# Performance work log

Hardware: AMD Instinct MI355X
Metric: run time of the kernel (lower is better)

## Reference

```python
import math
import jax, jax.numpy as jnp
import numpy as np

B, DIM, H = 16, 1024, 16
HD = DIM // H                      # 64
P_ORIG = 1024                      # num_patches arg
NP = math.ceil(math.sqrt(P_ORIG)) ** 2 // 2   # 512 attended tokens
ALPHA, BETA, GAMMA = 1.9, 3.8, 15.2           # iRPE euc config, ratio=1.9
NUM_BUCKETS = 2 * int(BETA) + 1               # 7


def _rp_bucket(L):
    """Static euclidean-distance relative-position buckets (iRPE 'euc')."""
    E = int(math.ceil(math.sqrt(L)))
    flat = np.arange(E * E)
    pos = np.stack([flat // E, flat % E], axis=1)[:L].astype(np.float64)  # [L,2]
    diff = pos[:, None, :] - pos[None, :, :]
    dis = np.round(np.sqrt((diff ** 2).sum(-1)))
    far = np.round(ALPHA + np.log(np.maximum(dis, 1e-9) / ALPHA)
                   / math.log(GAMMA / ALPHA) * (BETA - ALPHA))
    idx = np.where(dis <= ALPHA, np.round(dis), np.minimum(far, BETA)).astype(np.int32)
    idx = idx - idx.min()
    return jnp.asarray(idx)  # [L,L] int32 in [0, int(BETA)]

RP_BUCKET = _rp_bucket(NP)


def setup_inputs() -> dict:
    key = jax.random.key(0)
    ks = jax.random.split(key, 7)
    s = 0.02
    return {
        "x": jax.random.normal(ks[0], (B, P_ORIG, DIM), dtype=jnp.float32),
        "wq": jax.random.normal(ks[1], (DIM, DIM), dtype=jnp.float32) * s,
        "wk": jax.random.normal(ks[2], (DIM, DIM), dtype=jnp.float32) * s,
        "wv": jax.random.normal(ks[3], (DIM, DIM), dtype=jnp.float32) * s,
        "rpe_w": jax.random.normal(ks[4], (HD, NUM_BUCKETS), dtype=jnp.float32) * s,
        "proj_w": jax.random.normal(ks[5], (DIM, DIM), dtype=jnp.float32) * s,
        "proj_b": jax.random.normal(ks[6], (DIM,), dtype=jnp.float32) * s,
    }


def reference(x, wq, wk, wv, rpe_w, proj_w, proj_b):
    # F.pad on token axis with pad = NP - N (negative => crop)
    pad = NP - x.shape[1]
    if pad >= 0:
        x = jnp.pad(x, ((0, 0), (0, pad), (0, 0)))
    else:
        x = x[:, :NP, :]
    b = x.shape[0]
    scale = HD ** (-0.5)

    def heads(t):  # [b,NP,DIM] -> [b,H,NP,HD]
        return t.reshape(b, NP, H, HD).transpose(0, 2, 1, 3)

    q = heads(x @ wq.T)
    k = heads(x @ wk.T)
    v = heads(x @ wv.T)

    attn = jnp.einsum('bhid,bhjd->bhij', q, k) * scale
    # contextual RPE on keys (transposed): bias[b,h,i,j] = q[b,h,i,:] . W[:, bucket[i,j]]
    lt = jnp.einsum('bhid,dn->bhin', q, rpe_w)                 # [b,H,NP,NB]
    bias = jnp.take_along_axis(lt, RP_BUCKET[None, None, :, :], axis=3)  # [b,H,NP,NP]
    attn = jax.nn.softmax(attn + bias, axis=-1)

    out = jnp.einsum('bhij,bhjd->bhid', attn, v)
    out = out.transpose(0, 2, 1, 3).reshape(b, NP, DIM)
    out = out @ proj_w.T + proj_b
    return out[:, :P_ORIG, :]
```

## Files before the change

kernel.cpp:

```cpp
#include <hip/hip_runtime.h>

typedef __attribute__((ext_vector_type(8))) __bf16 bf16x8;
typedef __attribute__((ext_vector_type(4))) float f32x4;

#define DEVI static __device__ __forceinline__

DEVI unsigned short f2bf(float f) {
  unsigned int u = __float_as_uint(f);
  u += 0x7fffu + ((u >> 16) & 1u);
  return (unsigned short)(u >> 16);
}
DEVI float bf2f(unsigned short s) {
  return __uint_as_float(((unsigned int)s) << 16);
}

union Frag {
  bf16x8 v;
  __bf16 hf[8];
  unsigned short h[8];
  unsigned int w[4];
};

typedef __attribute__((address_space(1))) const void gv_t;
typedef __attribute__((address_space(3))) void sv_t;
#define GLOAD_LDS16(gp, lp) __builtin_amdgcn_global_load_lds((gv_t*)(gp), (sv_t*)(lp), 16, 0, 0)

#define QSCALE 0.18033688011112042f

__global__ __launch_bounds__(256) void k_prep(
    const float* __restrict__ x, const float* __restrict__ wq,
    const float* __restrict__ wk, const float* __restrict__ wv,
    const float* __restrict__ pw,
    unsigned short* __restrict__ xb, unsigned short* __restrict__ wb,
    unsigned char* __restrict__ bkt)
{
  int t = blockIdx.x * 256 + threadIdx.x;
  if (t >= 1572864) {
    int q = t - 1572864;
    int i = q >> 9, j = q & 511;
    int ir = i / 23, ic = i - ir * 23;
    int jr = j / 23, jc = j - jr * 23;
    int dy = ir - jr, dx = ic - jc;
    double dis = rint(sqrt((double)(dy * dy + dx * dx)));
    int v;
    if (dis <= 1.9) {
      v = (int)rint(dis);
    } else {
      double far = rint(1.9 + log(dis / 1.9) * (1.9 / log(8.0)));
      v = (int)fmin(far, 3.8);
    }
    bkt[q] = (unsigned char)v;
    return;
  }
  const float* src;
  unsigned short* dst;
  if (t < 1048576) {
    long e0 = (long)t << 3;
    int m = (int)(e0 >> 10), cc = (int)(e0 & 1023);
    int b = m >> 9, i = m & 511;
    src = x + (((long)(b << 10) + i) << 10) + cc;
    dst = xb + ((long)m << 10) + cc;
  } else {
    long e0 = (long)(t - 1048576) << 3;
    int mat = (int)(e0 >> 20);
    long off = e0 & 1048575;
    const float* s = (mat == 0) ? wq : (mat == 1) ? wk : (mat == 2) ? wv : pw;
    src = s + off;
    dst = wb + e0;
  }
  float4 a = *(const float4*)src;
  float4 b4 = *(const float4*)(src + 4);
  uint4 o;
  o.x = f2bf(a.x)  | ((unsigned)f2bf(a.y)  << 16);
  o.y = f2bf(a.z)  | ((unsigned)f2bf(a.w)  << 16);
  o.z = f2bf(b4.x) | ((unsigned)f2bf(b4.y) << 16);
  o.w = f2bf(b4.z) | ((unsigned)f2bf(b4.w) << 16);
  *(uint4*)dst = o;
}

__global__ __launch_bounds__(512) void k_gemm8(
    const unsigned short* __restrict__ A,
    const unsigned short* __restrict__ Bw,
    unsigned short* __restrict__ qh, unsigned short* __restrict__ kh,
    unsigned short* __restrict__ vt)
{
  __shared__ unsigned short sL[2 * 28672];

  const int bid = blockIdx.x;
  const int swz = (bid & 7) * 64 + (bid >> 3);
  const int tileN = swz & 15, tileM = swz >> 4;

  const int t = threadIdx.x;
  const int w = t >> 6, lane = t & 63;
  const int g4 = lane >> 4, c = lane & 15;
  const int wm = w >> 2, wn = w & 3;

  const char* lbase = (const char*)sL;
  const int acb = c * 64 + ((g4 * 16) ^ ((c & 8) ? 32 : 0));
  const int aoffbase = wm * 8192 + acb;
  int boff[3][2];
#pragma unroll
  for (int ni = 0; ni < 3; ++ni) {
    int row = wn * 48 + ni * 16 + c;
    int base = 32768 + (row >> 6) * 8192 + (row & 63) * 128;
    int rx = row & 7;
#pragma unroll
    for (int kk = 0; kk < 2; ++kk)
      boff[ni][kk] = base + (((kk * 4 + g4) ^ rx) << 4);
  }

  const int rowa = w * 16 + (lane >> 2);
  const int cola = ((lane & 3) * 8) ^ (((lane >> 2) & 8) ? 16 : 0);
  const unsigned short* sAp = A + (long)(tileM * 256 + rowa) * 1024 + cola;
  char* ldsta = (char*)sL + t * 16;
  const int rowbb = t >> 3;
  const int colbb = ((t & 7) ^ ((t >> 3) & 7)) * 8;
  const unsigned short* sBp = Bw + (long)(tileN * 192 + rowbb) * 1024 + colbb;
  char* ldstb = (char*)sL + 32768 + t * 16;

#define STGA(rh, kh, kn, ob) \
  GLOAD_LDS16(sAp + (long)(kn) * 64 + (rh) * 131072 + (kh) * 32, \
              ldsta + (ob) + (kh) * 16384 + (rh) * 8192)
#define STGB(gg, kn, ob) \
  GLOAD_LDS16(sBp + (long)(kn) * 64 + (gg) * 65536, \
              ldstb + (ob) + (gg) * 8192)

  f32x4 acc[8][3] = {};

  STGA(0, 0, 0, 0); STGA(1, 0, 0, 0);
  STGB(0, 0, 0); STGB(1, 0, 0); STGB(2, 0, 0);
  STGA(0, 1, 0, 0); STGA(1, 1, 0, 0);

#pragma unroll 1
  for (int kt = 0; kt < 16; ++kt) {
    const int cb = (kt & 1) ? 57344 : 0;
    const int ob = cb ^ 57344;
    const int kn = (kt < 15) ? kt + 1 : 15;

    {
      asm volatile("s_waitcnt vmcnt(2)" ::: "memory");
      __builtin_amdgcn_s_barrier();
      bf16x8 aa[4], bbf[3];
#pragma unroll
      for (int q = 0; q < 4; ++q)
        aa[q] = *(const bf16x8*)(lbase + cb + aoffbase + q * 1024);
#pragma unroll
      for (int ni = 0; ni < 3; ++ni)
        bbf[ni] = *(const bf16x8*)(lbase + cb + boff[ni][0]);
      STGA(0, 0, kn, ob); STGA(1, 0, kn, ob); STGB(0, kn, ob);
      __builtin_amdgcn_s_setprio(1);
#pragma unroll
      for (int mi = 0; mi < 4; ++mi)
#pragma unroll
        for (int ni = 0; ni < 3; ++ni)
          acc[mi][ni] = __builtin_amdgcn_mfma_f32_16x16x32_bf16(aa[mi], bbf[ni], acc[mi][ni], 0, 0, 0);
      __builtin_amdgcn_s_setprio(0);
      bf16x8 a2[4];
#pragma unroll
      for (int q = 0; q < 4; ++q)
        a2[q] = *(const bf16x8*)(lbase + cb + aoffbase + (4 + q) * 1024);
      STGB(1, kn, ob); STGB(2, kn, ob);
      __builtin_amdgcn_s_setprio(1);
#pragma unroll
      for (int mi = 0; mi < 4; ++mi)
#pragma unroll
        for (int ni = 0; ni < 3; ++ni)
          acc[4 + mi][ni] = __builtin_amdgcn_mfma_f32_16x16x32_bf16(a2[mi], bbf[ni], acc[4 + mi][ni], 0, 0, 0);
      __builtin_amdgcn_s_setprio(0);
    }
    {
      asm volatile("s_waitcnt vmcnt(5)" ::: "memory");
      __builtin_amdgcn_s_barrier();
      bf16x8 aa[4], bbf[3];
#pragma unroll
      for (int q = 0; q < 4; ++q)
        aa[q] = *(const bf16x8*)(lbase + cb + 16384 + aoffbase + q * 1024);
#pragma unroll
      for (int ni = 0; ni < 3; ++ni)
        bbf[ni] = *(const bf16x8*)(lbase + cb + boff[ni][1]);
      STGA(0, 1, kn, ob);
      __builtin_amdgcn_s_setprio(1);
#pragma unroll
      for (int mi = 0; mi < 4; ++mi)
#pragma unroll
        for (int ni = 0; ni < 3; ++ni)
          acc[mi][ni] = __builtin_amdgcn_mfma_f32_16x16x32_bf16(aa[mi], bbf[ni], acc[mi][ni], 0, 0, 0);
      __builtin_amdgcn_s_setprio(0);
      bf16x8 a2[4];
#pragma unroll
      for (int q = 0; q < 4; ++q)
        a2[q] = *(const bf16x8*)(lbase + cb + 16384 + aoffbase + (4 + q) * 1024);
      STGA(1, 1, kn, ob);
      __builtin_amdgcn_s_setprio(1);
#pragma unroll
      for (int mi = 0; mi < 4; ++mi)
#pragma unroll
        for (int ni = 0; ni < 3; ++ni)
          acc[4 + mi][ni] = __builtin_amdgcn_mfma_f32_16x16x32_bf16(a2[mi], bbf[ni], acc[4 + mi][ni], 0, 0, 0);
      __builtin_amdgcn_s_setprio(0);
    }
  }
  asm volatile("s_waitcnt vmcnt(0)" ::: "memory");
#undef STGA
#undef STGB

  const int m0 = tileM * 256 + wm * 128;
  const int n0 = tileN * 192 + wn * 48;
#pragma unroll
  for (int mi = 0; mi < 8; ++mi) {
    int mrow = m0 + mi * 16 + g4 * 4;
    int b = mrow >> 9, i = mrow & 511;
#pragma unroll
    for (int ni = 0; ni < 3; ++ni) {
      int n = n0 + ni * 16 + c;
      int mat = n >> 10;
      int cc = n & 1023;
      int h = cc >> 6, d = cc & 63;
      long bh = (long)(b * 16 + h);
      if (mat == 2) {
        unsigned int w0 = f2bf(acc[mi][ni][0]) | ((unsigned)f2bf(acc[mi][ni][1]) << 16);
        unsigned int w1 = f2bf(acc[mi][ni][2]) | ((unsigned)f2bf(acc[mi][ni][3]) << 16);
        *(uint2*)(vt + (bh * 64 + d) * 512 + i) = make_uint2(w0, w1);
      } else {
        float sc = (mat == 0) ? QSCALE : 1.0f;
        unsigned short* dst = (mat == 0 ? qh : kh) + (bh * 512 + i) * 64 + d;
#pragma unroll
        for (int r = 0; r < 4; ++r)
          dst[(long)r * 64] = f2bf(acc[mi][ni][r] * sc);
      }
    }
  }
}

__global__ __launch_bounds__(512) void k_gemm_proj(
    const unsigned short* __restrict__ A,
    const unsigned short* __restrict__ Bw,
    float* __restrict__ out, const float* __restrict__ bias)
{
  __shared__ unsigned short sL[3 * 12288];

  const int bid = blockIdx.x;
  const int swz = (bid & 7) * 32 + (bid >> 3);
  const int tileN = swz % 8, tileM = swz / 8;

  const int tid = threadIdx.x;
  const int w = tid >> 6, lane = tid & 63;
  const int g = lane >> 4, c = lane & 15;
  const int wm = w >> 1, wn = w & 1;

  const int sk = (g * 8) ^ ((c & 8) ? 16 : 0);
  int offA[4], offB[4];
#pragma unroll
  for (int i = 0; i < 4; ++i) {
    offA[i] = (wm * 4 + i) * 512 + c * 32 + sk;
    offB[i] = 8192 + (wn * 4 + i) * 512 + c * 32 + sk;
  }

  const int colb = ((lane & 3) * 8) ^ ((lane >= 32) ? 16 : 0);
  const unsigned short* gA0 = A  + ((long)(tileM * 256 + w * 32 + (lane >> 2))) * 1024 + colb;
  const unsigned short* gA1 = gA0 + 16 * 1024;
  const unsigned short* gB0 = Bw + ((long)(tileN * 128 + w * 16 + (lane >> 2))) * 1024 + colb;

#define STAGE(ktile, buf) do {                                             \
    const long ko_ = (long)(ktile) * 32;                                   \
    char* base_ = (char*)sL + (buf) * 24576;                               \
    GLOAD_LDS16(gA0 + ko_, base_ + (w * 2) * 1024 + lane * 16);            \
    GLOAD_LDS16(gA1 + ko_, base_ + (w * 2 + 1) * 1024 + lane * 16);        \
    GLOAD_LDS16(gB0 + ko_, base_ + 16384 + w * 1024 + lane * 16);          \
  } while (0)

  f32x4 acc[4][4] = {};

  STAGE(0, 0);
  STAGE(1, 1);

  int rb = 0, wbuf = 2;
  for (int t = 0; t < 32; ++t) {
    asm volatile("s_waitcnt vmcnt(3)" ::: "memory");
    __builtin_amdgcn_s_barrier();
    int kt = t + 2; if (kt > 31) kt = 31;
    STAGE(kt, wbuf);

    const unsigned short* lb = sL + rb * 12288;
    bf16x8 af[4], bf[4];
#pragma unroll
    for (int i = 0; i < 4; ++i) af[i] = *(const bf16x8*)(lb + offA[i]);
#pragma unroll
    for (int i = 0; i < 4; ++i) bf[i] = *(const bf16x8*)(lb + offB[i]);

    __builtin_amdgcn_s_setprio(1);
#pragma unroll
    for (int mi = 0; mi < 4; ++mi)
#pragma unroll
      for (int ni = 0; ni < 4; ++ni)
        acc[mi][ni] = __builtin_amdgcn_mfma_f32_16x16x32_bf16(af[mi], bf[ni], acc[mi][ni], 0, 0, 0);
    __builtin_amdgcn_s_setprio(0);
    asm volatile("s_waitcnt lgkmcnt(0)" ::: "memory");

    rb = (rb == 2) ? 0 : rb + 1;
    wbuf = (wbuf == 2) ? 0 : wbuf + 1;
  }
  asm volatile("s_waitcnt vmcnt(0)" ::: "memory");
#undef STAGE

  const int m0 = tileM * 256 + wm * 64;
  const int n0 = tileN * 128 + wn * 64;
#pragma unroll
  for (int mi = 0; mi < 4; ++mi) {
    int mrow = m0 + mi * 16 + g * 4;
#pragma unroll
    for (int ni = 0; ni < 4; ++ni) {
      int n = n0 + ni * 16 + c;
      float bv = bias[n];
#pragma unroll
      for (int r = 0; r < 4; ++r)
        out[(long)(mrow + r) * 1024 + n] = acc[mi][ni][r] + bv;
    }
  }
}

__global__ __launch_bounds__(512) void k_attn(
    const unsigned short* __restrict__ qh, const unsigned short* __restrict__ kh,
    const unsigned short* __restrict__ vt, const float* __restrict__ rpe,
    const unsigned char* __restrict__ bkt, unsigned short* __restrict__ ao)
{
  __shared__ float lt_lds[512 * 9];
  const int head = blockIdx.x;
  const int b = head >> 4, h = head & 15;
  const int w = threadIdx.x >> 6, lane = threadIdx.x & 63;
  const int g = lane >> 4, c = lane & 15;
  const int qbase = w * 64;
  const unsigned short* Q = qh + (long)head * 512 * 64;
  const unsigned short* K = kh + (long)head * 512 * 64;
  const unsigned short* V = vt + (long)head * 64 * 512;

  Frag qu[4][2];
#pragma unroll
  for (int it = 0; it < 4; ++it)
#pragma unroll
    for (int kk = 0; kk < 2; ++kk)
      qu[it][kk].v = *(const bf16x8*)(Q + (qbase + it * 16 + c) * 64 + kk * 32 + g * 8);

  float lt[4][7] = {};
#pragma unroll
  for (int kk = 0; kk < 2; ++kk)
#pragma unroll
    for (int tt = 0; tt < 8; ++tt) {
      int d = kk * 32 + g * 8 + tt;
      const float* rr = rpe + d * 7;
      float r0 = rr[0], r1 = rr[1], r2 = rr[2], r3 = rr[3], r4 = rr[4], r5 = rr[5], r6 = rr[6];
#pragma unroll
      for (int it = 0; it < 4; ++it) {
        float qv = bf2f(qu[it][kk].h[tt]);
        lt[it][0] += qv * r0; lt[it][1] += qv * r1; lt[it][2] += qv * r2;
        lt[it][3] += qv * r3; lt[it][4] += qv * r4; lt[it][5] += qv * r5;
        lt[it][6] += qv * r6;
      }
    }
#pragma unroll
  for (int it = 0; it < 4; ++it)
#pragma unroll
    for (int n = 0; n < 7; ++n) {
      float v = lt[it][n];
      v += __shfl_xor(v, 16);
      v += __shfl_xor(v, 32);
      if (g == 0) lt_lds[(qbase + it * 16 + c) * 9 + n] = v * 8.0f;
    }

  int rowb36[4];
  const unsigned char* bktp[4];
#pragma unroll
  for (int it = 0; it < 4; ++it) {
    int row = qbase + it * 16 + c;
    rowb36[it] = row * 36;
    bktp[it] = bkt + (long)row * 512 + g * 8;
  }

  f32x4 oacc[4][4] = {};
  float lp[4] = {0.f, 0.f, 0.f, 0.f};
  const int jperm = (c >> 2) * 8 + (c & 3);

  for (int jb = 0; jb < 512; jb += 32) {
    const int jp0 = jb + jperm;
    Frag kf[2][2];
#pragma unroll
    for (int jt = 0; jt < 2; ++jt)
#pragma unroll
      for (int kk = 0; kk < 2; ++kk)
        kf[jt][kk].v = *(const bf16x8*)(K + (jp0 + jt * 4) * 64 + kk * 32 + g * 8);

    uint2 bb[4];
#pragma unroll
    for (int it = 0; it < 4; ++it)
      bb[it] = *(const uint2*)(bktp[it] + jb);

    f32x4 s[2][4];
#pragma unroll
    for (int jt = 0; jt < 2; ++jt)
#pragma unroll
      for (int it = 0; it < 4; ++it) {
        f32x4 z = {0.f, 0.f, 0.f, 0.f};
        z = __builtin_amdgcn_mfma_f32_16x16x32_bf16(kf[jt][0].v, qu[it][0].v, z, 0, 0, 0);
        s[jt][it] = __builtin_amdgcn_mfma_f32_16x16x32_bf16(kf[jt][1].v, qu[it][1].v, z, 0, 0, 0);
      }

    Frag pfr[4];
#pragma unroll
    for (int it = 0; it < 4; ++it) {
      float ps = 0.f;
#pragma unroll
      for (int jt = 0; jt < 2; ++jt) {
        unsigned int bw = jt ? bb[it].y : bb[it].x;
#pragma unroll
        for (int r = 0; r < 4; ++r) {
          int bno = (bw >> (8 * r)) & 255;
          float bias = *(const float*)((const char*)lt_lds + rowb36[it] + (bno << 2));
          float sv = s[jt][it][r] + bias;
          float p;
          asm("v_exp_f32 %0, %1" : "=v"(p) : "v"(sv));
          ps += p;
          pfr[it].hf[jt * 4 + r] = (__bf16)p;
        }
      }
      lp[it] += ps;
    }

    bf16x8 vf[4];
#pragma unroll
    for (int dt = 0; dt < 4; ++dt)
      vf[dt] = *(const bf16x8*)(V + (dt * 16 + c) * 512 + jb + g * 8);

#pragma unroll
    for (int dt = 0; dt < 4; ++dt)
#pragma unroll
      for (int it = 0; it < 4; ++it)
        oacc[dt][it] = __builtin_amdgcn_mfma_f32_16x16x32_bf16(vf[dt], pfr[it].v, oacc[dt][it], 0, 0, 0);
  }

  float li[4];
#pragma unroll
  for (int it = 0; it < 4; ++it) {
    float v = lp[it];
    v += __shfl_xor(v, 16);
    v += __shfl_xor(v, 32);
    li[it] = 1.0f / v;
  }
#pragma unroll
  for (int dt = 0; dt < 4; ++dt)
#pragma unroll
    for (int it = 0; it < 4; ++it) {
      int irow = qbase + it * 16 + c;
      int d0 = dt * 16 + g * 4;
      unsigned int w0 = f2bf(oacc[dt][it][0] * li[it]) | ((unsigned)f2bf(oacc[dt][it][1] * li[it]) << 16);
      unsigned int w1 = f2bf(oacc[dt][it][2] * li[it]) | ((unsigned)f2bf(oacc[dt][it][3] * li[it]) << 16);
      *(uint2*)(ao + ((long)(b * 512 + irow)) * 1024 + h * 64 + d0) = make_uint2(w0, w1);
    }
}

extern "C" void kernel_launch(void* const* d_in, const int* in_sizes, int n_in,
                              void* d_out, int out_size, void* d_ws, size_t ws_size,
                              hipStream_t stream) {
  const float* x   = (const float*)d_in[0];
  const float* wq  = (const float*)d_in[1];
  const float* wk  = (const float*)d_in[2];
  const float* wv  = (const float*)d_in[3];
  const float* rpe = (const float*)d_in[4];
  const float* pw  = (const float*)d_in[5];
  const float* pb  = (const float*)d_in[6];
  float* out = (float*)d_out;

  char* ws = (char*)d_ws;
  unsigned short* xb  = (unsigned short*)(ws);
  unsigned short* wb  = (unsigned short*)(ws + 16777216);
  unsigned short* qhp = (unsigned short*)(ws + 25165824);
  unsigned short* khp = (unsigned short*)(ws + 41943040);
  unsigned short* vtp = (unsigned short*)(ws + 58720256);
  unsigned char*  bkt = (unsigned char*)(ws + 75497472);
  unsigned short* aop = xb;

  k_prep<<<dim3(7168), dim3(256), 0, stream>>>(x, wq, wk, wv, pw, xb, wb, bkt);
  k_gemm8<<<dim3(512), dim3(512), 0, stream>>>(xb, wb, qhp, khp, vtp);
  k_attn<<<dim3(256), dim3(512), 0, stream>>>(qhp, khp, vtp, rpe, bkt, aop);
  k_gemm_proj<<<dim3(256), dim3(512), 0, stream>>>(aop, wb + 3 * 1048576, out, pb);
}
```

Measured before the change: 154.5 us.

## Split attention key range across two wave groups and merge partials via LDS

Doubles the attention block to 1024 threads, with each half processing half of the keys for the same 512 queries. The second half writes its unnormalized output accumulators and row sums to shared memory, and the first half combines them, normalizes and stores the result. This aims to raise wave occupancy per CU, since only 256 blocks exist. The cost is a large LDS buffer, extra syncs and a reduction step, and the register budget per thread shrinks under the 1024-thread launch bound.

After: 261.9 us. 69.6% more time.

```diff
diff --git a/kernel.cpp b/kernel.cpp
--- a/kernel.cpp
+++ b/kernel.cpp
@@ -319,17 +319,20 @@
   }
 }
 
-__global__ __launch_bounds__(512) void k_attn(
+__global__ __launch_bounds__(1024) void k_attn(
     const unsigned short* __restrict__ qh, const unsigned short* __restrict__ kh,
     const unsigned short* __restrict__ vt, const float* __restrict__ rpe,
     const unsigned char* __restrict__ bkt, unsigned short* __restrict__ ao)
 {
+  __shared__ float pbuf[8 * 4352];
   __shared__ float lt_lds[512 * 9];
+  __shared__ float lsum_lds[512];
   const int head = blockIdx.x;
   const int b = head >> 4, h = head & 15;
   const int w = threadIdx.x >> 6, lane = threadIdx.x & 63;
+  const int qw = w & 7, seg = w >> 3;
   const int g = lane >> 4, c = lane & 15;
-  const int qbase = w * 64;
+  const int qbase = qw * 64;
   const unsigned short* Q = qh + (long)head * 512 * 64;
   const unsigned short* K = kh + (long)head * 512 * 64;
   const unsigned short* V = vt + (long)head * 64 * 512;
@@ -341,31 +344,34 @@
     for (int kk = 0; kk < 2; ++kk)
       qu[it][kk].v = *(const bf16x8*)(Q + (qbase + it * 16 + c) * 64 + kk * 32 + g * 8);
 
-  float lt[4][7] = {};
-#pragma unroll
-  for (int kk = 0; kk < 2; ++kk)
-#pragma unroll
-    for (int tt = 0; tt < 8; ++tt) {
-      int d = kk * 32 + g * 8 + tt;
-      const float* rr = rpe + d * 7;
-      float r0 = rr[0], r1 = rr[1], r2 = rr[2], r3 = rr[3], r4 = rr[4], r5 = rr[5], r6 = rr[6];
-#pragma unroll
-      for (int it = 0; it < 4; ++it) {
-        float qv = bf2f(qu[it][kk].h[tt]);
-        lt[it][0] += qv * r0; lt[it][1] += qv * r1; lt[it][2] += qv * r2;
-        lt[it][3] += qv * r3; lt[it][4] += qv * r4; lt[it][5] += qv * r5;
-        lt[it][6] += qv * r6;
+  if (seg == 0) {
+    float lt[4][7] = {};
+#pragma unroll
+    for (int kk = 0; kk < 2; ++kk)
+#pragma unroll
+      for (int tt = 0; tt < 8; ++tt) {
+        int d = kk * 32 + g * 8 + tt;
+        const float* rr = rpe + d * 7;
+        float r0 = rr[0], r1 = rr[1], r2 = rr[2], r3 = rr[3], r4 = rr[4], r5 = rr[5], r6 = rr[6];
+#pragma unroll
+        for (int it = 0; it < 4; ++it) {
+          float qv = bf2f(qu[it][kk].h[tt]);
+          lt[it][0] += qv * r0; lt[it][1] += qv * r1; lt[it][2] += qv * r2;
+          lt[it][3] += qv * r3; lt[it][4] += qv * r4; lt[it][5] += qv * r5;
+          lt[it][6] += qv * r6;
+        }
       }
-    }
-#pragma unroll
-  for (int it = 0; it < 4; ++it)
-#pragma unroll
-    for (int n = 0; n < 7; ++n) {
-      float v = lt[it][n];
-      v += __shfl_xor(v, 16);
-      v += __shfl_xor(v, 32);
-      if (g == 0) lt_lds[(qbase + it * 16 + c) * 9 + n] = v * 8.0f;
-    }
+#pragma unroll
+    for (int it = 0; it < 4; ++it)
+#pragma unroll
+      for (int n = 0; n < 7; ++n) {
+        float v = lt[it][n];
+        v += __shfl_xor(v, 16);
+        v += __shfl_xor(v, 32);
+        if (g == 0) lt_lds[(qbase + it * 16 + c) * 9 + n] = v * 8.0f;
+      }
+  }
+  __syncthreads();
 
   int rowb36[4];
   const unsigned char* bktp[4];
@@ -379,8 +385,9 @@
   f32x4 oacc[4][4] = {};
   float lp[4] = {0.f, 0.f, 0.f, 0.f};
   const int jperm = (c >> 2) * 8 + (c & 3);
-
-  for (int jb = 0; jb < 512; jb += 32) {
+  const int jb0 = seg * 256;
+
+  for (int jb = jb0; jb < jb0 + 256; jb += 32) {
     const int jp0 = jb + jperm;
     Frag kf[2][2];
 #pragma unroll
@@ -437,24 +444,47 @@
         oacc[dt][it] = __builtin_amdgcn_mfma_f32_16x16x32_bf16(vf[dt], pfr[it].v, oacc[dt][it], 0, 0, 0);
   }
 
-  float li[4];
+  float ls[4];
 #pragma unroll
   for (int it = 0; it < 4; ++it) {
     float v = lp[it];
     v += __shfl_xor(v, 16);
     v += __shfl_xor(v, 32);
-    li[it] = 1.0f / v;
-  }
-#pragma unroll
-  for (int dt = 0; dt < 4; ++dt)
-#pragma unroll
-    for (int it = 0; it < 4; ++it) {
-      int irow = qbase + it * 16 + c;
-      int d0 = dt * 16 + g * 4;
-      unsigned int w0 = f2bf(oacc[dt][it][0] * li[it]) | ((unsigned)f2bf(oacc[dt][it][1] * li[it]) << 16);
-      unsigned int w1 = f2bf(oacc[dt][it][2] * li[it]) | ((unsigned)f2bf(oacc[dt][it][3] * li[it]) << 16);
-      *(uint2*)(ao + ((long)(b * 512 + irow)) * 1024 + h * 64 + d0) = make_uint2(w0, w1);
-    }
+    ls[it] = v;
+  }
+
+  float* pw_ = pbuf + qw * 4352;
+  if (seg == 1) {
+#pragma unroll
+    for (int dt = 0; dt < 4; ++dt)
+#pragma unroll
+      for (int it = 0; it < 4; ++it)
+        *(f32x4*)(pw_ + (it * 16 + c) * 68 + dt * 16 + g * 4) = oacc[dt][it];
+    if (g == 0) {
+#pragma unroll
+      for (int it = 0; it < 4; ++it)
+        lsum_lds[qbase + it * 16 + c] = ls[it];
+    }
+  }
+  __syncthreads();
+  if (seg == 0) {
+    float li[4];
+#pragma unroll
+    for (int it = 0; it < 4; ++it)
+      li[it] = 1.0f / (ls[it] + lsum_lds[qbase + it * 16 + c]);
+#pragma unroll
+    for (int dt = 0; dt < 4; ++dt)
+#pragma unroll
+      for (int it = 0; it < 4; ++it) {
+        f32x4 o2 = *(const f32x4*)(pw_ + (it * 16 + c) * 68 + dt * 16 + g * 4);
+        f32x4 ov = (oacc[dt][it] + o2) * li[it];
+        int irow = qbase + it * 16 + c;
+        int d0 = dt * 16 + g * 4;
+        unsigned int w0 = f2bf(ov[0]) | ((unsigned)f2bf(ov[1]) << 16);
+        unsigned int w1 = f2bf(ov[2]) | ((unsigned)f2bf(ov[3]) << 16);
+        *(uint2*)(ao + ((long)(b * 512 + irow)) * 1024 + h * 64 + d0) = make_uint2(w0, w1);
+      }
+  }
 }
 
 extern "C" void kernel_launch(void* const* d_in, const int* in_sizes, int n_in,
@@ -480,6 +510,6 @@
 
   k_prep<<<dim3(7168), dim3(256), 0, stream>>>(x, wq, wk, wv, pw, xb, wb, bkt);
   k_gemm8<<<dim3(512), dim3(512), 0, stream>>>(xb, wb, qhp, khp, vtp);
-  k_attn<<<dim3(256), dim3(512), 0, stream>>>(qhp, khp, vtp, rpe, bkt, aop);
+  k_attn<<<dim3(256), dim3(1024), 0, stream>>>(qhp, khp, vtp, rpe, bkt, aop);
   k_gemm_proj<<<dim3(256), dim3(512), 0, stream>>>(aop, wb + 3 * 1048576, out, pb);
 }
```

## Split attention over key halves and merge partial outputs in a new kernel

Applied to the files above, without the earlier changes.

The attention kernel now launches twice as many blocks, each covering half the keys, so the 256-block grid is spread across more compute units. Unnormalized partial outputs and row sums go to scratch space, reusing the xb workspace and the output buffer, and a new merge kernel adds the halves and normalizes. The inner loop is also restructured to process one key subtile at a time, to reduce register pressure under the new occupancy hint. The cost is an extra launch, a full read and write of the attention output, and an extra bf16 rounding of the partial sums.

Result: slower. 302.0 us (+95.5%).

```diff
diff --git a/kernel.cpp b/kernel.cpp
--- a/kernel.cpp
+++ b/kernel.cpp
@@ -319,13 +319,16 @@
   }
 }
 
-__global__ __launch_bounds__(512) void k_attn(
+__global__ __launch_bounds__(512, 4) void k_attn_split(
     const unsigned short* __restrict__ qh, const unsigned short* __restrict__ kh,
     const unsigned short* __restrict__ vt, const float* __restrict__ rpe,
-    const unsigned char* __restrict__ bkt, unsigned short* __restrict__ ao)
+    const unsigned char* __restrict__ bkt,
+    unsigned short* __restrict__ po0, unsigned short* __restrict__ po1,
+    float* __restrict__ ls0, float* __restrict__ ls1)
 {
   __shared__ float lt_lds[512 * 9];
-  const int head = blockIdx.x;
+  const int bid = blockIdx.x;
+  const int head = bid >> 1, kvh = bid & 1;
   const int b = head >> 4, h = head & 15;
   const int w = threadIdx.x >> 6, lane = threadIdx.x & 63;
   const int g = lane >> 4, c = lane & 15;
@@ -333,6 +336,8 @@
   const unsigned short* Q = qh + (long)head * 512 * 64;
   const unsigned short* K = kh + (long)head * 512 * 64;
   const unsigned short* V = vt + (long)head * 64 * 512;
+  unsigned short* po = kvh ? po1 : po0;
+  float* ls = kvh ? ls1 : ls0;
 
   Frag qu[4][2];
 #pragma unroll
@@ -379,50 +384,39 @@
   f32x4 oacc[4][4] = {};
   float lp[4] = {0.f, 0.f, 0.f, 0.f};
   const int jperm = (c >> 2) * 8 + (c & 3);
-
-  for (int jb = 0; jb < 512; jb += 32) {
-    const int jp0 = jb + jperm;
-    Frag kf[2][2];
-#pragma unroll
-    for (int jt = 0; jt < 2; ++jt)
-#pragma unroll
-      for (int kk = 0; kk < 2; ++kk)
-        kf[jt][kk].v = *(const bf16x8*)(K + (jp0 + jt * 4) * 64 + kk * 32 + g * 8);
-
-    uint2 bb[4];
-#pragma unroll
-    for (int it = 0; it < 4; ++it)
-      bb[it] = *(const uint2*)(bktp[it] + jb);
-
-    f32x4 s[2][4];
-#pragma unroll
-    for (int jt = 0; jt < 2; ++jt)
+  const int jb0 = kvh * 256;
+
+  for (int jb = jb0; jb < jb0 + 256; jb += 32) {
+    Frag pfr[4];
+#pragma unroll
+    for (int jt = 0; jt < 2; ++jt) {
+      const int jp0 = jb + jperm + jt * 4;
+      Frag kf0, kf1;
+      kf0.v = *(const bf16x8*)(K + jp0 * 64 + g * 8);
+      kf1.v = *(const bf16x8*)(K + jp0 * 64 + 32 + g * 8);
+      f32x4 s[4];
 #pragma unroll
       for (int it = 0; it < 4; ++it) {
         f32x4 z = {0.f, 0.f, 0.f, 0.f};
-        z = __builtin_amdgcn_mfma_f32_16x16x32_bf16(kf[jt][0].v, qu[it][0].v, z, 0, 0, 0);
-        s[jt][it] = __builtin_amdgcn_mfma_f32_16x16x32_bf16(kf[jt][1].v, qu[it][1].v, z, 0, 0, 0);
+        z = __builtin_amdgcn_mfma_f32_16x16x32_bf16(kf0.v, qu[it][0].v, z, 0, 0, 0);
+        s[it] = __builtin_amdgcn_mfma_f32_16x16x32_bf16(kf1.v, qu[it][1].v, z, 0, 0, 0);
       }
-
-    Frag pfr[4];
-#pragma unroll
-    for (int it = 0; it < 4; ++it) {
-      float ps = 0.f;
-#pragma unroll
-      for (int jt = 0; jt < 2; ++jt) {
-        unsigned int bw = jt ? bb[it].y : bb[it].x;
+#pragma unroll
+      for (int it = 0; it < 4; ++it) {
+        unsigned int bw = *(const unsigned int*)(bktp[it] + jb + jt * 4);
+        float ps = 0.f;
 #pragma unroll
         for (int r = 0; r < 4; ++r) {
           int bno = (bw >> (8 * r)) & 255;
           float bias = *(const float*)((const char*)lt_lds + rowb36[it] + (bno << 2));
-          float sv = s[jt][it][r] + bias;
+          float sv = s[it][r] + bias;
           float p;
           asm("v_exp_f32 %0, %1" : "=v"(p) : "v"(sv));
           ps += p;
           pfr[it].hf[jt * 4 + r] = (__bf16)p;
         }
+        lp[it] += ps;
       }
-      lp[it] += ps;
     }
 
     bf16x8 vf[4];
@@ -437,24 +431,58 @@
         oacc[dt][it] = __builtin_amdgcn_mfma_f32_16x16x32_bf16(vf[dt], pfr[it].v, oacc[dt][it], 0, 0, 0);
   }
 
-  float li[4];
 #pragma unroll
   for (int it = 0; it < 4; ++it) {
     float v = lp[it];
     v += __shfl_xor(v, 16);
     v += __shfl_xor(v, 32);
-    li[it] = 1.0f / v;
-  }
+    if (g == 0) ls[head * 512 + qbase + it * 16 + c] = v;
+  }
+
 #pragma unroll
   for (int dt = 0; dt < 4; ++dt)
 #pragma unroll
     for (int it = 0; it < 4; ++it) {
       int irow = qbase + it * 16 + c;
       int d0 = dt * 16 + g * 4;
-      unsigned int w0 = f2bf(oacc[dt][it][0] * li[it]) | ((unsigned)f2bf(oacc[dt][it][1] * li[it]) << 16);
-      unsigned int w1 = f2bf(oacc[dt][it][2] * li[it]) | ((unsigned)f2bf(oacc[dt][it][3] * li[it]) << 16);
-      *(uint2*)(ao + ((long)(b * 512 + irow)) * 1024 + h * 64 + d0) = make_uint2(w0, w1);
-    }
+      unsigned int w0 = f2bf(oacc[dt][it][0]) | ((unsigned)f2bf(oacc[dt][it][1]) << 16);
+      unsigned int w1 = f2bf(oacc[dt][it][2]) | ((unsigned)f2bf(oacc[dt][it][3]) << 16);
+      *(uint2*)(po + ((long)(b * 512 + irow)) * 1024 + h * 64 + d0) = make_uint2(w0, w1);
+    }
+}
+
+__global__ __launch_bounds__(256) void k_merge(
+    const unsigned short* __restrict__ po1, const float* __restrict__ ls0,
+    const float* __restrict__ ls1, unsigned short* __restrict__ ao)
+{
+  int idx = blockIdx.x * 256 + threadIdx.x;
+  int m = idx >> 7;
+  int n0 = (idx & 127) << 3;
+  int head = (m >> 9) * 16 + (n0 >> 6);
+  int i = m & 511;
+  float li = 1.0f / (ls0[head * 512 + i] + ls1[head * 512 + i]);
+  long off = (long)m * 1024 + n0;
+  uint2 a = *(const uint2*)(ao + off);
+  uint2 bq = *(const uint2*)(po1 + off);
+  unsigned int r[2];
+#pragma unroll
+  for (int q = 0; q < 2; ++q) {
+    unsigned int ua = q ? a.y : a.x, ub = q ? bq.y : bq.x;
+    float f0 = (bf2f((unsigned short)(ua & 0xffff)) + bf2f((unsigned short)(ub & 0xffff))) * li;
+    float f1 = (bf2f((unsigned short)(ua >> 16)) + bf2f((unsigned short)(ub >> 16))) * li;
+    r[q] = f2bf(f0) | ((unsigned)f2bf(f1) << 16);
+  }
+  uint2 a2 = *(const uint2*)(ao + off + 4);
+  uint2 b2 = *(const uint2*)(po1 + off + 4);
+  unsigned int r2[2];
+#pragma unroll
+  for (int q = 0; q < 2; ++q) {
+    unsigned int ua = q ? a2.y : a2.x, ub = q ? b2.y : b2.x;
+    float f0 = (bf2f((unsigned short)(ua & 0xffff)) + bf2f((unsigned short)(ub & 0xffff))) * li;
+    float f1 = (bf2f((unsigned short)(ua >> 16)) + bf2f((unsigned short)(ub >> 16))) * li;
+    r2[q] = f2bf(f0) | ((unsigned)f2bf(f1) << 16);
+  }
+  *(uint4*)(ao + off) = make_uint4(r[0], r[1], r2[0], r2[1]);
 }
 
 extern "C" void kernel_launch(void* const* d_in, const int* in_sizes, int n_in,
@@ -476,10 +504,14 @@
   unsigned short* khp = (unsigned short*)(ws + 41943040);
   unsigned short* vtp = (unsigned short*)(ws + 58720256);
   unsigned char*  bkt = (unsigned char*)(ws + 75497472);
-  unsigned short* aop = xb;
+  unsigned short* po0 = xb;
+  unsigned short* po1 = (unsigned short*)d_out;
+  float* ls0 = (float*)((char*)d_out + 16777216);
+  float* ls1 = (float*)((char*)d_out + 17825792);
 
   k_prep<<<dim3(7168), dim3(256), 0, stream>>>(x, wq, wk, wv, pw, xb, wb, bkt);
   k_gemm8<<<dim3(512), dim3(512), 0, stream>>>(xb, wb, qhp, khp, vtp);
-  k_attn<<<dim3(256), dim3(512), 0, stream>>>(qhp, khp, vtp, rpe, bkt, aop);
-  k_gemm_proj<<<dim3(256), dim3(512), 0, stream>>>(aop, wb + 3 * 1048576, out, pb);
-}
+  k_attn_split<<<dim3(512), dim3(512), 0, stream>>>(qhp, khp, vtp, rpe, bkt, po0, po1, ls0, ls1);
+  k_merge<<<dim3(4096), dim3(256), 0, stream>>>(po1, ls0, ls1, po0);
+  k_gemm_proj<<<dim3(256), dim3(512), 0, stream>>>(po0, wb + 3 * 1048576, out, pb);
+}
```

## Stage K/V tiles through a triple-buffered LDS ring with async global-to-LDS loads

Applied to the files above, without the earlier changes.

The attention kernel now loads each 32-key block of K and V^T into a three-slot shared-memory ring using direct global-to-LDS loads, issued two iterations ahead. All 512 threads of the workgroup share each staged tile, with XOR-swizzled offsets to avoid bank conflicts. Previously all 8 waves fetched the same K/V data straight from global memory. This cuts redundant global traffic and hides latency, at the cost of a barrier per iteration, extra LDS use, and reliance on the GLOAD_LDS16 macro and waitcnt ordering being correct.

Result: faster. 148.4 us (-3.9%).

```diff
diff --git a/kernel.cpp b/kernel.cpp
--- a/kernel.cpp
+++ b/kernel.cpp
@@ -324,22 +324,48 @@
     const unsigned short* __restrict__ vt, const float* __restrict__ rpe,
     const unsigned char* __restrict__ bkt, unsigned short* __restrict__ ao)
 {
+  __shared__ char ring[3 * 8192];
   __shared__ float lt_lds[512 * 9];
   const int head = blockIdx.x;
   const int b = head >> 4, h = head & 15;
-  const int w = threadIdx.x >> 6, lane = threadIdx.x & 63;
+  const int t = threadIdx.x;
+  const int w = t >> 6, lane = t & 63;
   const int g = lane >> 4, c = lane & 15;
   const int qbase = w * 64;
   const unsigned short* Q = qh + (long)head * 512 * 64;
   const unsigned short* K = kh + (long)head * 512 * 64;
   const unsigned short* V = vt + (long)head * 64 * 512;
 
+  const unsigned short* sgp;
+  char* sld;
+  int sjstep;
+  if (t < 256) {
+    int row = t >> 3;
+    int chunk = (t & 7) ^ (row & 7);
+    sgp = K + (long)row * 64 + chunk * 8;
+    sld = ring + t * 16;
+    sjstep = 64;
+  } else {
+    int u = t - 256;
+    int row = u >> 2;
+    int chunk = (u & 3) ^ (row & 3);
+    sgp = V + (long)row * 512 + chunk * 8;
+    sld = ring + 4096 + u * 16;
+    sjstep = 1;
+  }
+
+#define STAGE(jt_, slot_) \
+  GLOAD_LDS16(sgp + (long)(jt_) * 32 * sjstep, sld + (slot_) * 8192)
+
   Frag qu[4][2];
 #pragma unroll
   for (int it = 0; it < 4; ++it)
 #pragma unroll
     for (int kk = 0; kk < 2; ++kk)
       qu[it][kk].v = *(const bf16x8*)(Q + (qbase + it * 16 + c) * 64 + kk * 32 + g * 8);
+
+  STAGE(0, 0);
+  STAGE(1, 1);
 
   float lt[4][7] = {};
 #pragma unroll
@@ -376,18 +402,42 @@
     bktp[it] = bkt + (long)row * 512 + g * 8;
   }
 
+  const int jperm = (c >> 2) * 8 + (c & 3);
+  int koff[2][2];
+#pragma unroll
+  for (int jt = 0; jt < 2; ++jt) {
+    int jp = jperm + jt * 4;
+#pragma unroll
+    for (int kk = 0; kk < 2; ++kk)
+      koff[jt][kk] = jp * 128 + (((kk * 4 + g) ^ (jp & 7)) << 4);
+  }
+  int voff[4];
+#pragma unroll
+  for (int dt = 0; dt < 4; ++dt) {
+    int r = dt * 16 + c;
+    voff[dt] = 4096 + r * 64 + ((g ^ (r & 3)) << 4);
+  }
+
   f32x4 oacc[4][4] = {};
   float lp[4] = {0.f, 0.f, 0.f, 0.f};
-  const int jperm = (c >> 2) * 8 + (c & 3);
-
-  for (int jb = 0; jb < 512; jb += 32) {
-    const int jp0 = jb + jperm;
+
+  int rb = 0, wbuf = 2;
+#pragma unroll 1
+  for (int kt = 0; kt < 16; ++kt) {
+    asm volatile("s_waitcnt vmcnt(1)" ::: "memory");
+    __builtin_amdgcn_s_barrier();
+    int kn = (kt < 14) ? kt + 2 : 15;
+    STAGE(kn, wbuf);
+
+    const char* lb = ring + rb * 8192;
+    const int jb = kt * 32;
+
     Frag kf[2][2];
 #pragma unroll
     for (int jt = 0; jt < 2; ++jt)
 #pragma unroll
       for (int kk = 0; kk < 2; ++kk)
-        kf[jt][kk].v = *(const bf16x8*)(K + (jp0 + jt * 4) * 64 + kk * 32 + g * 8);
+        kf[jt][kk].v = *(const bf16x8*)(lb + koff[jt][kk]);
 
     uint2 bb[4];
 #pragma unroll
@@ -428,14 +478,20 @@
     bf16x8 vf[4];
 #pragma unroll
     for (int dt = 0; dt < 4; ++dt)
-      vf[dt] = *(const bf16x8*)(V + (dt * 16 + c) * 512 + jb + g * 8);
+      vf[dt] = *(const bf16x8*)(lb + voff[dt]);
 
 #pragma unroll
     for (int dt = 0; dt < 4; ++dt)
 #pragma unroll
       for (int it = 0; it < 4; ++it)
         oacc[dt][it] = __builtin_amdgcn_mfma_f32_16x16x32_bf16(vf[dt], pfr[it].v, oacc[dt][it], 0, 0, 0);
-  }
+
+    asm volatile("s_waitcnt lgkmcnt(0)" ::: "memory");
+    rb = (rb == 2) ? 0 : rb + 1;
+    wbuf = (wbuf == 2) ? 0 : wbuf + 1;
+  }
+  asm volatile("s_waitcnt vmcnt(0)" ::: "memory");
+#undef STAGE
 
   float li[4];
 #pragma unroll
```
